# Kernel optimization log

Measured on AMD Instinct MI355X. Metric: run time of the kernel, lower is better.

## Reference

```python
import jax, jax.numpy as jnp
import numpy as np

D = 1024      # hidden_size
M = 256       # num_random_features
N = 16384     # number of hidden states
K = 8192      # number of weight rows (HSM nodes)
EPS = 1e-6


def _orthogonal_random_features(key, d, m):
    # m < d: single QR block, first m rows, scaled by sqrt(d)
    rm = jax.random.normal(key, (d, d), dtype=jnp.float32)
    q, _ = jnp.linalg.qr(rm)
    return q[:m] * jnp.sqrt(jnp.float32(d))


def setup_inputs() -> dict:
    key = jax.random.key(0)
    k1, k2, k3 = jax.random.split(key, 3)
    hidden_states = jax.random.normal(k1, (N, D), dtype=jnp.float32)
    weights = jax.random.normal(k2, (K, D), dtype=jnp.float32)
    omega = _orthogonal_random_features(k3, D, M)
    return {"hidden_states": hidden_states, "weights": weights, "omega": omega}


def _positive_random_features(x, omega):
    # phi(x) = (exp(x @ Omega^T - ||x||^2/2 - max) + eps) / sqrt(m)
    projection = x @ omega.T                                  # (..., m)
    x_norm_sq = jnp.sum(x * x, axis=-1, keepdims=True)        # (..., 1)
    exponent = projection - x_norm_sq / 2
    exponent_max = jnp.max(exponent, axis=-1, keepdims=True)
    features = (jnp.exp(exponent - exponent_max) + EPS) / jnp.sqrt(jnp.float32(omega.shape[0]))
    return features, x_norm_sq, exponent_max


def reference(hidden_states, weights, omega):
    # temperature = 1.0 (default), so no input rescaling
    phi_h, h_norm_sq, h_max = _positive_random_features(hidden_states, omega)  # (n,m)
    phi_w, w_norm_sq, w_max = _positive_random_features(weights, omega)        # (k,m)
    rf_kernel = phi_h @ phi_w.T                                                # (n,k)
    log_correction = (h_norm_sq + w_norm_sq.T) / 2 + h_max + w_max.T           # (n,k)
    log_correction = jnp.clip(log_correction, -80.0, 80.0)
    log_rf_kernel = jnp.log(rf_kernel + 1e-10)
    log_exp_approx = jnp.clip(log_rf_kernel + log_correction, -80.0, 80.0)
    exp_approx = jnp.exp(log_exp_approx)
    return exp_approx / (1.0 + exp_approx)
```

## Files before the change

kernel.cpp:

```cpp
#include <hip/hip_runtime.h>

#define DD 1024
#define MM 256
#define NN 16384
#define KK 8192

typedef float f32x4 __attribute__((ext_vector_type(4)));
typedef unsigned int u32x4 __attribute__((ext_vector_type(4)));
typedef unsigned int u32x2 __attribute__((ext_vector_type(2)));
typedef __bf16 bf16x8 __attribute__((ext_vector_type(8)));
typedef unsigned short u16;
typedef unsigned int u32;

static __device__ __forceinline__ u16 f2bf(float f) {
    u32 u = __builtin_bit_cast(u32, f);
    u32 r = u + 0x7fffu + ((u >> 16) & 1u);
    return (u16)(r >> 16);
}
static __device__ __forceinline__ float bf2f(u16 h) {
    u32 u = ((u32)h) << 16;
    return __builtin_bit_cast(float, u);
}

static __device__ __forceinline__ void gload_lds16(const void* g, void* l) {
    __builtin_amdgcn_global_load_lds(
        (const __attribute__((address_space(1))) u32*)g,
        (__attribute__((address_space(3))) u32*)l, 16, 0, 0);
}

static __device__ __forceinline__ bf16x8 ldfrag(const u16* p) {
    return __builtin_bit_cast(bf16x8, *(const u32x4*)p);
}

#define MFMA16(a, b, c) __builtin_amdgcn_mfma_f32_16x16x32_bf16((a), (b), (c), 0, 0, 0)

__global__ void k_conv(const float* __restrict__ om, u16* __restrict__ oh,
                       u16* __restrict__ ol) {
    int i = (blockIdx.x * blockDim.x + threadIdx.x) * 4;
    f32x4 x = *(const f32x4*)(om + i);
    ushort4 h, l;
    u16 t;
    t = f2bf(x.x); h.x = t; l.x = f2bf(x.x - bf2f(t));
    t = f2bf(x.y); h.y = t; l.y = f2bf(x.y - bf2f(t));
    t = f2bf(x.z); h.z = t; l.z = f2bf(x.z - bf2f(t));
    t = f2bf(x.w); h.w = t; l.w = f2bf(x.w - bf2f(t));
    *(ushort4*)(oh + i) = h;
    *(ushort4*)(ol + i) = l;
}

__global__ __launch_bounds__(256, 4)
void k_stageA(const float* __restrict__ Hs, const float* __restrict__ Ws,
              const u16* __restrict__ Oh, const u16* __restrict__ Ol,
              u16* __restrict__ phiH, u16* __restrict__ phiW,
              float* __restrict__ emH, float* __restrict__ emW)
{
    __shared__ alignas(16) u16 Ah[32 * 32];
    __shared__ alignas(16) u16 Al[32 * 32];
    __shared__ alignas(16) u16 Bh[256 * 32];
    __shared__ alignas(16) u16 Bl[256 * 32];
    __shared__ float redmax[4][32];

    const int tid  = threadIdx.x;
    const int lane = tid & 63;
    const int wid  = tid >> 6;

    const float* __restrict__ X;
    u16* __restrict__ phi;
    float* __restrict__ em;
    int row0;
    if (blockIdx.x < NN / 32) {
        X = Hs; phi = phiH; em = emH; row0 = blockIdx.x * 32;
    } else {
        X = Ws; phi = phiW; em = emW; row0 = (blockIdx.x - NN / 32) * 32;
    }

    f32x4 acc[2][4];
#pragma unroll
    for (int m = 0; m < 2; ++m)
#pragma unroll
        for (int n = 0; n < 4; ++n) acc[m][n] = f32x4{0.f, 0.f, 0.f, 0.f};

    const int arow = tid >> 3;
    const int acol = (tid & 7) * 4;
    const float* __restrict__ xrow = X + (long)(row0 + arow) * DD;
    const int a_idx = arow * 32 + (acol ^ (((arow >> 1) & 3) << 3));

    const int r16 = lane & 15;
    const int h8  = (lane >> 4) << 3;
    int aoffs[2], boffs[4];
#pragma unroll
    for (int m = 0; m < 2; ++m) {
        int row = m * 16 + r16;
        aoffs[m] = row * 32 + (h8 ^ (((row >> 1) & 3) << 3));
    }
#pragma unroll
    for (int n = 0; n < 4; ++n) {
        int row = wid * 64 + n * 16 + r16;
        boffs[n] = row * 32 + (h8 ^ (((row >> 1) & 3) << 3));
    }

    for (int ks = 0; ks < DD / 32; ++ks) {
        const int k0 = ks * 32;
#pragma unroll
        for (int s = 0; s < 4; ++s) {
            const int c    = s * 256 + tid;
            const int brow = c >> 2;
            const int scol = k0 + (((c & 3) << 3) ^ (((brow >> 1) & 3) << 3));
            gload_lds16(Oh + brow * DD + scol, Bh + (s * 256 + wid * 64) * 8);
            gload_lds16(Ol + brow * DD + scol, Bl + (s * 256 + wid * 64) * 8);
        }
        f32x4 x = *(const f32x4*)(xrow + k0 + acol);
        u32x2 ph, pl;
#pragma unroll
        for (int j = 0; j < 2; ++j) {
            u16 h0 = f2bf(x[2 * j]);
            u16 h1 = f2bf(x[2 * j + 1]);
            u16 l0 = f2bf(x[2 * j] - bf2f(h0));
            u16 l1 = f2bf(x[2 * j + 1] - bf2f(h1));
            ph[j] = (u32)h0 | ((u32)h1 << 16);
            pl[j] = (u32)l0 | ((u32)l1 << 16);
        }
        *(u32x2*)(Ah + a_idx) = ph;
        *(u32x2*)(Al + a_idx) = pl;
        __syncthreads();

        bf16x8 fah[2], fal[2], fbh[4], fbl[4];
#pragma unroll
        for (int m = 0; m < 2; ++m) {
            fah[m] = ldfrag(Ah + aoffs[m]);
            fal[m] = ldfrag(Al + aoffs[m]);
        }
#pragma unroll
        for (int n = 0; n < 4; ++n) {
            fbh[n] = ldfrag(Bh + boffs[n]);
            fbl[n] = ldfrag(Bl + boffs[n]);
        }
#pragma unroll
        for (int m = 0; m < 2; ++m)
#pragma unroll
            for (int n = 0; n < 4; ++n) {
                acc[m][n] = MFMA16(fah[m], fbh[n], acc[m][n]);
                acc[m][n] = MFMA16(fah[m], fbl[n], acc[m][n]);
                acc[m][n] = MFMA16(fal[m], fbh[n], acc[m][n]);
            }
        __syncthreads();
    }

#pragma unroll
    for (int m = 0; m < 2; ++m) {
#pragma unroll
        for (int i = 0; i < 4; ++i) {
            float v = fmaxf(fmaxf(acc[m][0][i], acc[m][1][i]),
                            fmaxf(acc[m][2][i], acc[m][3][i]));
            v = fmaxf(v, __shfl_xor(v, 1));
            v = fmaxf(v, __shfl_xor(v, 2));
            v = fmaxf(v, __shfl_xor(v, 4));
            v = fmaxf(v, __shfl_xor(v, 8));
            if (r16 == 0) redmax[wid][m * 16 + ((lane >> 4) << 2) + i] = v;
        }
    }
    __syncthreads();
    if (tid < 32) {
        float fm = fmaxf(fmaxf(redmax[0][tid], redmax[1][tid]),
                         fmaxf(redmax[2][tid], redmax[3][tid]));
        em[row0 + tid] = __expf(fminf(fmaxf(-fm, -87.f), 87.f));
    }
#pragma unroll
    for (int m = 0; m < 2; ++m) {
#pragma unroll
        for (int i = 0; i < 4; ++i) {
            const int rl = m * 16 + ((lane >> 4) << 2) + i;
            const float fm = fmaxf(fmaxf(redmax[0][rl], redmax[1][rl]),
                                   fmaxf(redmax[2][rl], redmax[3][rl]));
#pragma unroll
            for (int n = 0; n < 4; ++n) {
                float p   = acc[m][n][i];
                float ph_ = (__expf(p - fm) + 1e-6f) * 0.0625f;
                phi[(long)(row0 + rl) * MM + wid * 64 + n * 16 + r16] = f2bf(ph_);
            }
        }
    }
}

__global__ __launch_bounds__(256, 3)
void k_stageB(const u16* __restrict__ PH, const u16* __restrict__ PW,
              const float* __restrict__ EH, const float* __restrict__ EW,
              float* __restrict__ out)
{
    __shared__ alignas(16) unsigned char smem_raw[64 * 130 * 4];
    u16* const As = (u16*)smem_raw;
    u16* const Bs = As + 128 * 64;
    float* const ftile = (float*)smem_raw;
    const int FST = 130;

    const int tid  = threadIdx.x;
    const int lane = tid & 63;
    const int wid  = tid >> 6;
    const int bm   = blockIdx.x >> 6;
    const int bn   = blockIdx.x & 63;
    const int row0 = bm * 128, col0 = bn * 128;
    const int wr   = wid >> 1, wc = wid & 1;
    const int r16  = lane & 15;
    const int h8   = (lane >> 4) << 3;

    f32x4 acc[4][4];
#pragma unroll
    for (int m = 0; m < 4; ++m)
#pragma unroll
        for (int n = 0; n < 4; ++n) acc[m][n] = f32x4{0.f, 0.f, 0.f, 0.f};

    int aoffs[2][4], boffs[2][4];
#pragma unroll
    for (int sl = 0; sl < 2; ++sl) {
#pragma unroll
        for (int m = 0; m < 4; ++m) {
            int row = wr * 64 + m * 16 + r16;
            aoffs[sl][m] = row * 64 + (((((sl * 32 + h8) << 1)) ^ ((row & 7) << 4)) >> 1);
        }
#pragma unroll
        for (int n = 0; n < 4; ++n) {
            int row = wc * 64 + n * 16 + r16;
            boffs[sl][n] = row * 64 + (((((sl * 32 + h8) << 1)) ^ ((row & 7) << 4)) >> 1);
        }
    }

    for (int ks = 0; ks < 4; ++ks) {
        const int k0 = ks * 64;
#pragma unroll
        for (int s = 0; s < 4; ++s) {
            const int c    = s * 256 + tid;
            const int row  = c >> 3;
            const int cbl  = ((c & 7) << 4) ^ ((row & 7) << 4);
            const int scol = k0 + (cbl >> 1);
            gload_lds16(PH + (long)(row0 + row) * MM + scol, As + (s * 256 + wid * 64) * 8);
            gload_lds16(PW + (long)(col0 + row) * MM + scol, Bs + (s * 256 + wid * 64) * 8);
        }
        __syncthreads();
#pragma unroll
        for (int sl = 0; sl < 2; ++sl) {
            bf16x8 fa[4], fb[4];
#pragma unroll
            for (int m = 0; m < 4; ++m) fa[m] = ldfrag(As + aoffs[sl][m]);
#pragma unroll
            for (int n = 0; n < 4; ++n) fb[n] = ldfrag(Bs + boffs[sl][n]);
#pragma unroll
            for (int m = 0; m < 4; ++m)
#pragma unroll
                for (int n = 0; n < 4; ++n)
                    acc[m][n] = MFMA16(fa[m], fb[n], acc[m][n]);
        }
        __syncthreads();
    }

    float ew_[4];
#pragma unroll
    for (int n = 0; n < 4; ++n) ew_[n] = EW[col0 + wc * 64 + n * 16 + r16];

#pragma unroll
    for (int mm = 0; mm < 2; ++mm) {
        if (mm == 1) {
            asm volatile("s_waitcnt lgkmcnt(0)" ::: "memory");
            __builtin_amdgcn_s_barrier();
        }
#pragma unroll
        for (int ms = 0; ms < 2; ++ms) {
            const int m = 2 * mm + ms;
#pragma unroll
            for (int i = 0; i < 4; ++i) {
                const int lr   = wr * 32 + ms * 16 + ((lane >> 4) << 2) + i;
                const int grow = row0 + wr * 64 + m * 16 + ((lane >> 4) << 2) + i;
                const float eh = EH[grow];
#pragma unroll
                for (int n = 0; n < 4; ++n) {
                    float rf = acc[m][n][i] + 1e-10f;
                    float t  = eh * ew_[n];
                    float o  = rf * __builtin_amdgcn_rcpf(rf + t);
                    ftile[lr * FST + wc * 64 + n * 16 + r16] = o;
                }
            }
        }
        asm volatile("s_waitcnt lgkmcnt(0)" ::: "memory");
        __builtin_amdgcn_s_barrier();
#pragma unroll
        for (int p = 0; p < 8; ++p) {
            const int r = p * 8 + (tid >> 5);
            const int c = (tid & 31) * 4;
            f32x4 v = *(const f32x4*)&ftile[r * FST + c];
            const int grow = row0 + (r >> 5) * 64 + (2 * mm + ((r >> 4) & 1)) * 16 + (r & 15);
            __builtin_nontemporal_store(
                v, (f32x4*)(out + (long)grow * KK + col0 + c));
        }
    }
}

extern "C" void kernel_launch(void* const* d_in, const int* in_sizes, int n_in,
                              void* d_out, int out_size, void* d_ws, size_t ws_size,
                              hipStream_t stream) {
    (void)in_sizes; (void)n_in; (void)out_size; (void)ws_size;
    const float* H  = (const float*)d_in[0];
    const float* W  = (const float*)d_in[1];
    const float* Om = (const float*)d_in[2];
    float* out = (float*)d_out;

    char* ws   = (char*)d_ws;
    u16*  phiH = (u16*)ws;
    u16*  phiW = (u16*)(ws + (size_t)NN * MM * 2);
    float* emh = (float*)(ws + (size_t)(NN + KK) * MM * 2);
    float* emw = emh + NN;
    u16*  oh   = (u16*)(emw + KK);
    u16*  ol   = oh + MM * DD;

    k_conv<<<(MM * DD) / 1024, 256, 0, stream>>>(Om, oh, ol);
    k_stageA<<<(NN + KK) / 32, 256, 0, stream>>>(H, W, oh, ol, phiH, phiW, emh, emw);
    k_stageB<<<(NN / 128) * (KK / 128), 256, 0, stream>>>(phiH, phiW, emh, emw, out);
}
```

Before: 181.3 us.

## Load stage A MFMA fragments directly from global with register double buffering

Stage A no longer stages omega and input tiles through LDS with barriers. Each lane now loads its MFMA fragments straight from global memory into registers, using a two-deep register pipeline so loads for the next k-step overlap compute. Launch bounds are swapped: stage A drops to 3 waves per SIMD for the extra registers, and stage B rises to 4. Threads in a wave now fetch overlapping omega rows redundantly through cache instead of sharing via LDS, and the higher register pressure can limit occupancy.

```diff
diff --git a/kernel.cpp b/kernel.cpp
--- a/kernel.cpp
+++ b/kernel.cpp
@@ -48,21 +48,19 @@
     *(ushort4*)(ol + i) = l;
 }
 
-__global__ __launch_bounds__(256, 4)
+__global__ __launch_bounds__(256, 3)
 void k_stageA(const float* __restrict__ Hs, const float* __restrict__ Ws,
               const u16* __restrict__ Oh, const u16* __restrict__ Ol,
               u16* __restrict__ phiH, u16* __restrict__ phiW,
               float* __restrict__ emH, float* __restrict__ emW)
 {
-    __shared__ alignas(16) u16 Ah[32 * 32];
-    __shared__ alignas(16) u16 Al[32 * 32];
-    __shared__ alignas(16) u16 Bh[256 * 32];
-    __shared__ alignas(16) u16 Bl[256 * 32];
     __shared__ float redmax[4][32];
 
     const int tid  = threadIdx.x;
     const int lane = tid & 63;
     const int wid  = tid >> 6;
+    const int r16  = lane & 15;
+    const int h8   = (lane >> 4) << 3;
 
     const float* __restrict__ X;
     u16* __restrict__ phi;
@@ -80,70 +78,60 @@
 #pragma unroll
         for (int n = 0; n < 4; ++n) acc[m][n] = f32x4{0.f, 0.f, 0.f, 0.f};
 
-    const int arow = tid >> 3;
-    const int acol = (tid & 7) * 4;
-    const float* __restrict__ xrow = X + (long)(row0 + arow) * DD;
-    const int a_idx = arow * 32 + (acol ^ (((arow >> 1) & 3) << 3));
-
-    const int r16 = lane & 15;
-    const int h8  = (lane >> 4) << 3;
-    int aoffs[2], boffs[4];
-#pragma unroll
-    for (int m = 0; m < 2; ++m) {
-        int row = m * 16 + r16;
-        aoffs[m] = row * 32 + (h8 ^ (((row >> 1) & 3) << 3));
-    }
-#pragma unroll
-    for (int n = 0; n < 4; ++n) {
-        int row = wid * 64 + n * 16 + r16;
-        boffs[n] = row * 32 + (h8 ^ (((row >> 1) & 3) << 3));
-    }
-
-    for (int ks = 0; ks < DD / 32; ++ks) {
-        const int k0 = ks * 32;
-#pragma unroll
-        for (int s = 0; s < 4; ++s) {
-            const int c    = s * 256 + tid;
-            const int brow = c >> 2;
-            const int scol = k0 + (((c & 3) << 3) ^ (((brow >> 1) & 3) << 3));
-            gload_lds16(Oh + brow * DD + scol, Bh + (s * 256 + wid * 64) * 8);
-            gload_lds16(Ol + brow * DD + scol, Bl + (s * 256 + wid * 64) * 8);
-        }
-        f32x4 x = *(const f32x4*)(xrow + k0 + acol);
-        u32x2 ph, pl;
-#pragma unroll
-        for (int j = 0; j < 2; ++j) {
-            u16 h0 = f2bf(x[2 * j]);
-            u16 h1 = f2bf(x[2 * j + 1]);
-            u16 l0 = f2bf(x[2 * j] - bf2f(h0));
-            u16 l1 = f2bf(x[2 * j + 1] - bf2f(h1));
-            ph[j] = (u32)h0 | ((u32)h1 << 16);
-            pl[j] = (u32)l0 | ((u32)l1 << 16);
-        }
-        *(u32x2*)(Ah + a_idx) = ph;
-        *(u32x2*)(Al + a_idx) = pl;
-        __syncthreads();
-
-        bf16x8 fah[2], fal[2], fbh[4], fbl[4];
+    const u16*  obh = Oh + (long)(wid * 64 + r16) * DD + h8;
+    const u16*  obl = Ol + (long)(wid * 64 + r16) * DD + h8;
+    const float* xb = X + (long)(row0 + r16) * DD + h8;
+
+    u32x4 bh0[4], bl0[4], bh1[4], bl1[4];
+    f32x4 ax0[2][2], ax1[2][2];
+
+    auto load = [&](int k0, u32x4 (&bh)[4], u32x4 (&bl)[4], f32x4 (&ax)[2][2]) {
+#pragma unroll
+        for (int n = 0; n < 4; ++n) {
+            bh[n] = *(const u32x4*)(obh + n * 16 * DD + k0);
+            bl[n] = *(const u32x4*)(obl + n * 16 * DD + k0);
+        }
 #pragma unroll
         for (int m = 0; m < 2; ++m) {
-            fah[m] = ldfrag(Ah + aoffs[m]);
-            fal[m] = ldfrag(Al + aoffs[m]);
-        }
-#pragma unroll
-        for (int n = 0; n < 4; ++n) {
-            fbh[n] = ldfrag(Bh + boffs[n]);
-            fbl[n] = ldfrag(Bl + boffs[n]);
+            ax[m][0] = *(const f32x4*)(xb + m * 16 * DD + k0);
+            ax[m][1] = *(const f32x4*)(xb + m * 16 * DD + k0 + 4);
+        }
+    };
+    auto compute = [&](u32x4 (&bh)[4], u32x4 (&bl)[4], f32x4 (&ax)[2][2]) {
+        bf16x8 fah[2], fal[2];
+#pragma unroll
+        for (int m = 0; m < 2; ++m) {
+            const float e[8] = {ax[m][0][0], ax[m][0][1], ax[m][0][2], ax[m][0][3],
+                                ax[m][1][0], ax[m][1][1], ax[m][1][2], ax[m][1][3]};
+            u32x4 ph, pl;
+#pragma unroll
+            for (int j = 0; j < 4; ++j) {
+                u16 a0 = f2bf(e[2 * j]);
+                u16 a1 = f2bf(e[2 * j + 1]);
+                u16 c0 = f2bf(e[2 * j] - bf2f(a0));
+                u16 c1 = f2bf(e[2 * j + 1] - bf2f(a1));
+                ph[j] = (u32)a0 | ((u32)a1 << 16);
+                pl[j] = (u32)c0 | ((u32)c1 << 16);
+            }
+            fah[m] = __builtin_bit_cast(bf16x8, ph);
+            fal[m] = __builtin_bit_cast(bf16x8, pl);
         }
 #pragma unroll
         for (int m = 0; m < 2; ++m)
 #pragma unroll
             for (int n = 0; n < 4; ++n) {
-                acc[m][n] = MFMA16(fah[m], fbh[n], acc[m][n]);
-                acc[m][n] = MFMA16(fah[m], fbl[n], acc[m][n]);
-                acc[m][n] = MFMA16(fal[m], fbh[n], acc[m][n]);
+                acc[m][n] = MFMA16(fah[m], __builtin_bit_cast(bf16x8, bh[n]), acc[m][n]);
+                acc[m][n] = MFMA16(fah[m], __builtin_bit_cast(bf16x8, bl[n]), acc[m][n]);
+                acc[m][n] = MFMA16(fal[m], __builtin_bit_cast(bf16x8, bh[n]), acc[m][n]);
             }
-        __syncthreads();
+    };
+
+    load(0, bh0, bl0, ax0);
+    for (int ks = 0; ks < 32; ks += 2) {
+        load((ks + 1) * 32, bh1, bl1, ax1);
+        compute(bh0, bl0, ax0);
+        if (ks + 2 < 32) load((ks + 2) * 32, bh0, bl0, ax0);
+        compute(bh1, bl1, ax1);
     }
 
 #pragma unroll
@@ -182,7 +170,7 @@
     }
 }
 
-__global__ __launch_bounds__(256, 3)
+__global__ __launch_bounds__(256, 4)
 void k_stageB(const u16* __restrict__ PH, const u16* __restrict__ PW,
               const float* __restrict__ EH, const float* __restrict__ EW,
               float* __restrict__ out)
```

New measurement: 241.5 us. 33.2% more time.
